# Optimization experiments

Hardware: AMD Instinct MI355X
Metric: run time of the kernel (lower is better)

Reference implementation:

```python
import jax, jax.numpy as jnp
import numpy as np

N, E = 50000, 800000
F_NODE, F_EDGE, H, LAT, MAXN = 128, 16, 128, 64, 200


def setup_inputs() -> dict:
    key = jax.random.key(0)
    ks = jax.random.split(key, 40)
    s = 0.05
    p = {
        'x': jax.random.normal(ks[0], (N, F_NODE), jnp.float32),
        'edge_index': jax.random.randint(ks[1], (2, E), 0, N, jnp.int64),
        'edge_attr': jax.random.normal(ks[2], (E, F_EDGE), jnp.float32),
        'eps': jax.random.normal(ks[3], (1, LAT), jnp.float32),
        'num_nodes': N,
        # GATConv layer 1 (heads=1)
        'W1': jax.random.normal(ks[4], (F_NODE, H), jnp.float32) * s,
        'att_src1': jax.random.normal(ks[5], (H,), jnp.float32) * s,
        'att_dst1': jax.random.normal(ks[6], (H,), jnp.float32) * s,
        'We1': jax.random.normal(ks[7], (F_EDGE, H), jnp.float32) * s,
        'att_e1': jax.random.normal(ks[8], (H,), jnp.float32) * s,
        'b1': jnp.zeros((H,), jnp.float32),
        # GATConv layer 2
        'W2': jax.random.normal(ks[9], (H, H), jnp.float32) * s,
        'att_src2': jax.random.normal(ks[10], (H,), jnp.float32) * s,
        'att_dst2': jax.random.normal(ks[11], (H,), jnp.float32) * s,
        'We2': jax.random.normal(ks[12], (F_EDGE, H), jnp.float32) * s,
        'att_e2': jax.random.normal(ks[13], (H,), jnp.float32) * s,
        'b2': jnp.zeros((H,), jnp.float32),
        # heads
        'mu_W': jax.random.normal(ks[14], (H, LAT), jnp.float32) * s,
        'mu_b': jnp.zeros((LAT,), jnp.float32),
        'lv_W': jax.random.normal(ks[15], (H, LAT), jnp.float32) * s,
        'lv_b': jnp.zeros((LAT,), jnp.float32),
        'dec_W': jax.random.normal(ks[16], (LAT, H), jnp.float32) * s,
        'dec_b': jnp.zeros((H,), jnp.float32),
        'adj_W1': jax.random.normal(ks[17], (H, H), jnp.float32) * s,
        'adj_b1': jnp.zeros((H,), jnp.float32),
        'adj_W2': jax.random.normal(ks[18], (H, MAXN), jnp.float32) * s,
        'adj_b2': jnp.zeros((MAXN,), jnp.float32),
        'nd_W1': jax.random.normal(ks[19], (H, H), jnp.float32) * s,
        'nd_b1': jnp.zeros((H,), jnp.float32),
        'nd_W2': jax.random.normal(ks[20], (H, F_NODE), jnp.float32) * s,
        'nd_b2': jnp.zeros((F_NODE,), jnp.float32),
    }
    return p


def _gat(h, src, dst, ea, W, a_s, a_d, We, a_e, b, n):
    # PyG GATConv, heads=1: linear transform, per-edge attention, segment softmax over dst
    g = h @ W                                     # [n, H]
    alpha = jax.nn.leaky_relu((g @ a_s)[src] + (g @ a_d)[dst] + (ea @ We) @ a_e,
                              negative_slope=0.2)  # [E']
    m = jax.ops.segment_max(alpha, dst, num_segments=n)
    ex = jnp.exp(alpha - m[dst])
    den = jax.ops.segment_sum(ex, dst, num_segments=n)
    w = ex / den[dst]
    return jax.ops.segment_sum(w[:, None] * g[src], dst, num_segments=n) + b


def _forward(x, edge_index, edge_attr, eps, num_nodes,
             W1, att_src1, att_dst1, We1, att_e1, b1,
             W2, att_src2, att_dst2, We2, att_e2, b2,
             mu_W, mu_b, lv_W, lv_b, dec_W, dec_b,
             adj_W1, adj_b1, adj_W2, adj_b2, nd_W1, nd_b1, nd_W2, nd_b2):
    n = x.shape[0]
    src, dst = edge_index[0], edge_index[1]
    # add self loops; self-loop edge_attr = per-node mean of incoming edge_attr (PyG fill_value='mean')
    deg = jax.ops.segment_sum(jnp.ones((src.shape[0],), x.dtype), dst, num_segments=n)
    mean_ea = jax.ops.segment_sum(edge_attr, dst, num_segments=n) / jnp.maximum(deg, 1.0)[:, None]
    loop = jnp.arange(n)
    src_f = jnp.concatenate([src, loop])
    dst_f = jnp.concatenate([dst, loop])
    ea_f = jnp.concatenate([edge_attr, mean_ea])
    h = jax.nn.relu(_gat(x, src_f, dst_f, ea_f, W1, att_src1, att_dst1, We1, att_e1, b1, n))
    h = jax.nn.relu(_gat(h, src_f, dst_f, ea_f, W2, att_src2, att_dst2, We2, att_e2, b2, n))
    hg = h.mean(axis=0, keepdims=True)            # global_mean_pool, single graph -> [1, H]
    mu = hg @ mu_W + mu_b
    logvar = hg @ lv_W + lv_b
    z = mu + eps * jnp.exp(0.5 * logvar)
    hd = jax.nn.relu(z @ dec_W + dec_b)           # [1, H]
    hn = jnp.broadcast_to(hd[:, None, :], (1, num_nodes, hd.shape[-1]))
    adj = jax.nn.relu(hn @ adj_W1 + adj_b1) @ adj_W2 + adj_b2   # [1, n, MAXN]
    adj = adj[:, :, :num_nodes]
    nodes = jax.nn.relu(hn @ nd_W1 + nd_b1) @ nd_W2 + nd_b2     # [1, n, F_NODE]
    return adj, nodes, mu, logvar


def reference(x, edge_index, edge_attr, eps, num_nodes,
              W1, att_src1, att_dst1, We1, att_e1, b1,
              W2, att_src2, att_dst2, We2, att_e2, b2,
              mu_W, mu_b, lv_W, lv_b, dec_W, dec_b,
              adj_W1, adj_b1, adj_W2, adj_b2, nd_W1, nd_b1, nd_W2, nd_b2):
    return _forward(x, edge_index, edge_attr, eps, num_nodes,
                    W1, att_src1, att_dst1, We1, att_e1, b1,
                    W2, att_src2, att_dst2, We2, att_e2, b2,
                    mu_W, mu_b, lv_W, lv_b, dec_W, dec_b,
                    adj_W1, adj_b1, adj_W2, adj_b2, nd_W1, nd_b1, nd_W2, nd_b2)
```

## Files before the change

### kernel.cpp

```cpp
#include <hip/hip_runtime.h>
#include <math.h>

#define NN   50000
#define EE   800000
#define EF   850000
#define HH   128
#define FE   16
#define LATD 64
#define MAXNN 200

#define ADJ_TOT   10000000
#define NODES_TOT 6400000
#define OUT_TOT   16400000
#define MU_OFF    16400000
#define LV_OFF    16400064

typedef __attribute__((ext_vector_type(8))) short bf16x8;
typedef __attribute__((ext_vector_type(4))) float f32x4;

__device__ __forceinline__ unsigned short f2bf(float f){
  unsigned int u = __float_as_uint(f);
  unsigned int r = (u + 0x7FFFu + ((u>>16)&1u)) >> 16;
  return (unsigned short)r;
}
__device__ __forceinline__ float bf2f(unsigned short h){
  return __uint_as_float(((unsigned int)h)<<16);
}

__global__ void kinit(int* ideg, float* hgsum){
  int i = blockIdx.x*blockDim.x + threadIdx.x;
  if(i < NN) ideg[i]=0;
  if(i < HH) hgsum[i]=0.f;
}

__global__ void kwa(const float* We1, const float* ae1, const float* We2, const float* ae2,
                    float* wa1, float* wa2){
  int t = threadIdx.x;
  if(t < FE){
    float s1=0.f, s2=0.f;
    for(int j=0;j<HH;j++){ s1 += We1[t*HH+j]*ae1[j]; s2 += We2[t*HH+j]*ae2[j]; }
    wa1[t]=s1; wa2[t]=s2;
  }
}

__global__ void kwprep(const float* __restrict__ W1, const float* __restrict__ W2,
                       unsigned short* __restrict__ Wp1, unsigned short* __restrict__ Wp2){
  int t = blockIdx.x*256 + threadIdx.x;
  if(t < HH*HH){
    int n = t >> 7, k = t & 127;
    Wp1[t] = f2bf(W1[k*HH + n]);
    Wp2[t] = f2bf(W2[k*HH + n]);
  }
}

__global__ void kdeg(const int* __restrict__ ei, int* ideg, int* __restrict__ erank){
  int e = blockIdx.x*blockDim.x + threadIdx.x;
  if(e<EE) erank[e] = atomicAdd(&ideg[ei[EE+e]], 1);
}

__global__ void kscan1(const int* __restrict__ ideg, int* rowstart, int* blocksum){
  __shared__ int sd[1024];
  int t=threadIdx.x; int i=blockIdx.x*1024+t;
  int v = (i<NN)? (ideg[i]+1) : 0;
  sd[t]=v; __syncthreads();
  for(int off=1; off<1024; off<<=1){
    int x = (t>=off)? sd[t-off] : 0;
    __syncthreads();
    sd[t] += x;
    __syncthreads();
  }
  if(i<NN) rowstart[i] = sd[t]-v;
  if(t==1023) blocksum[blockIdx.x]=sd[1023];
}
__global__ void kscan2(const int* blocksum, int* blockoff, int nb){
  if(threadIdx.x==0){
    int run=0;
    for(int b=0;b<nb;b++){ blockoff[b]=run; run+=blocksum[b]; }
    blockoff[nb]=run;
  }
}
__global__ void kscan3(int* rowstart, const int* __restrict__ blockoff, int nb){
  int i=blockIdx.x*blockDim.x+threadIdx.x;
  if(i<NN) rowstart[i]+=blockoff[i>>10];
  if(i==0) rowstart[NN]=blockoff[nb];
}

__global__ void kscatter(const int* __restrict__ ei, const float* __restrict__ ea,
                         const float* __restrict__ wa1, const float* __restrict__ wa2,
                         const int* __restrict__ rowstart, const int* __restrict__ erank,
                         float4* __restrict__ csr){
  int e=blockIdx.x*blockDim.x+threadIdx.x;
  if(e>=EE) return;
  int s=ei[e], d=ei[EE+e];
  const float4* ea4 = (const float4*)(ea + (size_t)e*FE);
  float4 v0=ea4[0], v1=ea4[1], v2=ea4[2], v3=ea4[3];
  float va[16]={v0.x,v0.y,v0.z,v0.w, v1.x,v1.y,v1.z,v1.w,
                v2.x,v2.y,v2.z,v2.w, v3.x,v3.y,v3.z,v3.w};
  float d1=0.f,d2=0.f;
  #pragma unroll
  for(int f=0;f<FE;f++){ d1+=va[f]*wa1[f]; d2+=va[f]*wa2[f]; }
  int pos = rowstart[d] + erank[e];
  csr[pos] = make_float4(__int_as_float(s), d1, d2, 0.f);
}

__global__ __launch_bounds__(256) void kself(const int* __restrict__ rowstart,
                      const int* __restrict__ ideg,
                      float4* __restrict__ csr){
  int tid = threadIdx.x;
  int l16 = tid & 15;
  int grp = tid >> 4;
  int i = blockIdx.x*16 + grp;
  if(i>=NN) return;
  int base = rowstart[i]; int deg = ideg[i];
  float s1=0.f, s2=0.f;
  for(int k=l16;k<deg;k+=16){ float4 en=csr[base+k]; s1+=en.y; s2+=en.z; }
  #pragma unroll
  for(int m=8;m>=1;m>>=1){ s1+=__shfl_xor(s1,m,16); s2+=__shfl_xor(s2,m,16); }
  if(l16==0){
    float dg = (float)deg; if(dg<1.f) dg=1.f;
    csr[base+deg] = make_float4(__int_as_float(i), s1/dg, s2/dg, 0.f);
  }
}

__global__ __launch_bounds__(256) void kgemm3(const void* __restrict__ hin, int h_is_fp32,
    const unsigned short* __restrict__ Wp,
    const float* __restrict__ atts, const float* __restrict__ attd,
    unsigned short* __restrict__ Gbf, float* __restrict__ asrc, float* __restrict__ adst){
  int lane = threadIdx.x & 63;
  int wid  = threadIdx.x >> 6;
  int l = lane & 15, q = lane >> 4;
  int r0 = blockIdx.x*64 + wid*16;
  if(r0 >= NN) return;
  const unsigned short* hb = (const unsigned short*)hin;
  const float*          hf = (const float*)hin;
  int row = r0 + l;

  f32x4 acc[8];
  #pragma unroll
  for(int t=0;t<8;t++) acc[t]=(f32x4){0.f,0.f,0.f,0.f};

  #pragma unroll
  for(int kb=0;kb<4;kb++){
    bf16x8 a;
    if(h_is_fp32){
      const float* p = hf + (size_t)row*HH + kb*32 + q*8;
      float4 u0 = *(const float4*)(p);
      float4 u1 = *(const float4*)(p+4);
      a[0]=(short)f2bf(u0.x); a[1]=(short)f2bf(u0.y); a[2]=(short)f2bf(u0.z); a[3]=(short)f2bf(u0.w);
      a[4]=(short)f2bf(u1.x); a[5]=(short)f2bf(u1.y); a[6]=(short)f2bf(u1.z); a[7]=(short)f2bf(u1.w);
    } else {
      a = *(const bf16x8*)(hb + (size_t)row*HH + kb*32 + q*8);
    }
    #pragma unroll
    for(int t=0;t<8;t++){
      bf16x8 b = *(const bf16x8*)(Wp + (size_t)(t*16+l)*HH + kb*32 + q*8);
      acc[t] = __builtin_amdgcn_mfma_f32_16x16x32_bf16(a, b, acc[t], 0,0,0);
    }
  }

  float av[8], dv[8];
  #pragma unroll
  for(int t=0;t<8;t++){ av[t]=atts[t*16+l]; dv[t]=attd[t*16+l]; }
  #pragma unroll
  for(int reg=0;reg<4;reg++){
    float ps=0.f, pd=0.f;
    #pragma unroll
    for(int t=0;t<8;t++){ ps+=acc[t][reg]*av[t]; pd+=acc[t][reg]*dv[t]; }
    #pragma unroll
    for(int m=8;m>=1;m>>=1){ ps+=__shfl_xor(ps,m,16); pd+=__shfl_xor(pd,m,16); }
    if(l==0){ int R=r0+q*4+reg; asrc[R]=ps; adst[R]=pd; }
  }
  #pragma unroll
  for(int t=0;t<8;t++)
    #pragma unroll
    for(int reg=0;reg<4;reg++)
      Gbf[(size_t)(r0+q*4+reg)*HH + t*16 + l] = f2bf(acc[t][reg]);
}

__global__ __launch_bounds__(256) void kgat(const unsigned short* __restrict__ A,
    const float* __restrict__ asrc, const float* __restrict__ adst,
    const int* __restrict__ rowstart, const float4* __restrict__ csr,
    int etsel, const float* __restrict__ bias,
    float* __restrict__ alphabuf, int* __restrict__ srcbuf,
    unsigned short* __restrict__ Bout){
  int lane = threadIdx.x & 63;
  int wid  = threadIdx.x >> 6;
  int i = blockIdx.x*4 + wid;
  if(i >= NN) return;
  int base = rowstart[i]; int len = rowstart[i+1]-base;
  float adi = adst[i];
  float acc0=0.f, acc1=0.f;
  float den;
  if(__builtin_expect(len <= 64, 1)){
    float a = -1e30f; int s=0;
    if(lane < len){
      float4 en = csr[base+lane];
      s = __float_as_int(en.x);
      float et = etsel ? en.z : en.y;
      a = asrc[s] + adi + et;
      a = a>0.f ? a : 0.2f*a;
    }
    float m = a;
    #pragma unroll
    for(int mk=32;mk>=1;mk>>=1) m = fmaxf(m, __shfl_xor(m, mk));
    float ex = (lane<len) ? __expf(a-m) : 0.f;
    float sm = ex;
    #pragma unroll
    for(int mk=32;mk>=1;mk>>=1) sm += __shfl_xor(sm, mk);
    den = sm;
    const unsigned short* Ap = A + lane*2;
    int k=0;
    for(; k+4<=len; k+=4){
      float wk0=__shfl(ex,k+0); int sk0=__shfl(s,k+0);
      float wk1=__shfl(ex,k+1); int sk1=__shfl(s,k+1);
      float wk2=__shfl(ex,k+2); int sk2=__shfl(s,k+2);
      float wk3=__shfl(ex,k+3); int sk3=__shfl(s,k+3);
      unsigned p0 = *(const unsigned*)(Ap + (size_t)sk0*HH);
      unsigned p1 = *(const unsigned*)(Ap + (size_t)sk1*HH);
      unsigned p2 = *(const unsigned*)(Ap + (size_t)sk2*HH);
      unsigned p3 = *(const unsigned*)(Ap + (size_t)sk3*HH);
      acc0 += wk0 * __uint_as_float(p0<<16);
      acc1 += wk0 * __uint_as_float(p0 & 0xFFFF0000u);
      acc0 += wk1 * __uint_as_float(p1<<16);
      acc1 += wk1 * __uint_as_float(p1 & 0xFFFF0000u);
      acc0 += wk2 * __uint_as_float(p2<<16);
      acc1 += wk2 * __uint_as_float(p2 & 0xFFFF0000u);
      acc0 += wk3 * __uint_as_float(p3<<16);
      acc1 += wk3 * __uint_as_float(p3 & 0xFFFF0000u);
    }
    for(; k<len; k++){
      float wk = __shfl(ex, k);
      int   sk = __shfl(s, k);
      unsigned pr = *(const unsigned*)(Ap + (size_t)sk*HH);
      acc0 += wk * __uint_as_float(pr<<16);
      acc1 += wk * __uint_as_float(pr & 0xFFFF0000u);
    }
  } else {
    float lm = -1e30f;
    for(int k=lane;k<len;k+=64){
      float4 en = csr[base+k];
      int s = __float_as_int(en.x);
      float et = etsel ? en.z : en.y;
      float a = asrc[s] + adi + et;
      a = a>0.f ? a : 0.2f*a;
      alphabuf[base+k]=a; srcbuf[base+k]=s;
      lm = fmaxf(lm,a);
    }
    #pragma unroll
    for(int mk=32;mk>=1;mk>>=1) lm = fmaxf(lm, __shfl_xor(lm, mk));
    float ls=0.f;
    for(int k=lane;k<len;k+=64){
      float ex = __expf(alphabuf[base+k]-lm);
      alphabuf[base+k]=ex; ls+=ex;
    }
    #pragma unroll
    for(int mk=32;mk>=1;mk>>=1) ls += __shfl_xor(ls, mk);
    den = ls;
    for(int c=0;c<len;c+=64){
      int kk = c+lane;
      float w = (kk<len)? alphabuf[base+kk] : 0.f;
      int   s = (kk<len)? srcbuf[base+kk] : 0;
      int lim = min(64, len-c);
      for(int j=0;j<lim;j++){
        float wk = __shfl(w, j);
        int   sk = __shfl(s, j);
        unsigned pr = *(const unsigned*)(A + (size_t)sk*HH + lane*2);
        acc0 += wk * __uint_as_float(pr<<16);
        acc1 += wk * __uint_as_float(pr & 0xFFFF0000u);
      }
    }
  }
  float inv = 1.f/den;
  float2 bb = *(const float2*)(bias + lane*2);
  float ox = fmaxf(acc0*inv + bb.x, 0.f);
  float oy = fmaxf(acc1*inv + bb.y, 0.f);
  unsigned ov = (unsigned)f2bf(ox) | ((unsigned)f2bf(oy)<<16);
  *(unsigned*)(Bout + (size_t)i*HH + lane*2) = ov;
}

__global__ __launch_bounds__(256) void khg(const unsigned short* __restrict__ B, float* hgsum){
  int f = threadIdx.x & 127;
  int half = threadIdx.x >> 7;
  float s=0.f;
  for(int i = blockIdx.x*2+half; i < NN; i += gridDim.x*2)
    s += bf2f(B[(size_t)i*HH + f]);
  __shared__ float sd[256];
  sd[threadIdx.x]=s; __syncthreads();
  if(half==0) atomicAdd(&hgsum[f], sd[threadIdx.x]+sd[threadIdx.x+128]);
}

__global__ __launch_bounds__(256) void kdec(const float* __restrict__ hgsum, const float* __restrict__ eps,
   const float* muW,const float* mub,const float* lvW,const float* lvb,
   const float* decW,const float* decb,
   const float* aW1,const float* ab1,const float* aW2,const float* ab2,
   const float* nW1,const float* nb1,const float* nW2,const float* nb2,
   float* out, float* rowadj, float* rownodes){
  __shared__ float hg[HH], z[LATD], hd[HH], t1[HH], t2[HH];
  int t=threadIdx.x;
  if(t<HH) hg[t]=hgsum[t]*(1.0f/NN);
  __syncthreads();
  if(t<LATD){
    float mu=mub[t], lv=lvb[t];
    for(int k=0;k<HH;k++){ mu += hg[k]*muW[k*LATD+t]; lv += hg[k]*lvW[k*LATD+t]; }
    out[MU_OFF+t]=mu; out[LV_OFF+t]=lv;
    z[t]=mu + eps[t]*expf(0.5f*lv);
  }
  __syncthreads();
  if(t<HH){
    float a=decb[t];
    for(int k=0;k<LATD;k++) a += z[k]*decW[k*HH+t];
    hd[t]=fmaxf(a,0.f);
  }
  __syncthreads();
  if(t<HH){
    float a=ab1[t];
    for(int k=0;k<HH;k++) a += hd[k]*aW1[k*HH+t];
    t1[t]=fmaxf(a,0.f);
  } else {
    int j=t-HH;
    float a=nb1[j];
    for(int k=0;k<HH;k++) a += hd[k]*nW1[k*HH+j];
    t2[j]=fmaxf(a,0.f);
  }
  __syncthreads();
  for(int j=t;j<MAXNN;j+=256){
    float a=ab2[j];
    for(int k=0;k<HH;k++) a += t1[k]*aW2[k*MAXNN+j];
    rowadj[j]=a;
  }
  if(t<HH){
    float a=nb2[t];
    for(int k=0;k<HH;k++) a += t2[k]*nW2[k*HH+t];
    rownodes[t]=a;
  }
}

__global__ __launch_bounds__(256) void kbcast(const float* __restrict__ rowadj,
                                              const float* __restrict__ rownodes,
                                              float* __restrict__ out){
  __shared__ float row[MAXNN+HH];
  int t=threadIdx.x;
  if(t<MAXNN) row[t]=rowadj[t];
  if(t<HH) row[MAXNN+t]=rownodes[t];
  __syncthreads();
  int stride=gridDim.x*blockDim.x;
  for(int idx=blockIdx.x*blockDim.x+t; idx<OUT_TOT; idx+=stride){
    if(idx<ADJ_TOT) out[idx]=row[idx%MAXNN];
    else { int j=(idx-ADJ_TOT)&(HH-1); out[idx]=row[MAXNN+j]; }
  }
}

extern "C" void kernel_launch(void* const* d_in, const int* in_sizes, int n_in,
                              void* d_out, int out_size, void* d_ws, size_t ws_size,
                              hipStream_t stream){
  const float* x   = (const float*)d_in[0];
  const int*   ei  = (const int*)d_in[1];
  const float* ea  = (const float*)d_in[2];
  const float* eps = (const float*)d_in[3];
  const float* W1  =(const float*)d_in[5];
  const float* as1 =(const float*)d_in[6];
  const float* ad1 =(const float*)d_in[7];
  const float* We1 =(const float*)d_in[8];
  const float* ae1 =(const float*)d_in[9];
  const float* b1  =(const float*)d_in[10];
  const float* W2  =(const float*)d_in[11];
  const float* as2 =(const float*)d_in[12];
  const float* ad2 =(const float*)d_in[13];
  const float* We2 =(const float*)d_in[14];
  const float* ae2 =(const float*)d_in[15];
  const float* b2  =(const float*)d_in[16];
  const float* muW =(const float*)d_in[17];
  const float* mub =(const float*)d_in[18];
  const float* lvW =(const float*)d_in[19];
  const float* lvb =(const float*)d_in[20];
  const float* decW=(const float*)d_in[21];
  const float* decb=(const float*)d_in[22];
  const float* aW1 =(const float*)d_in[23];
  const float* ab1 =(const float*)d_in[24];
  const float* aW2 =(const float*)d_in[25];
  const float* ab2 =(const float*)d_in[26];
  const float* nW1 =(const float*)d_in[27];
  const float* nb1 =(const float*)d_in[28];
  const float* nW2 =(const float*)d_in[29];
  const float* nb2 =(const float*)d_in[30];
  float* out=(float*)d_out;

  char* w=(char*)d_ws;
  unsigned short* Abf = (unsigned short*)w; w += (size_t)NN*HH*2;
  unsigned short* Bbf = (unsigned short*)w; w += (size_t)NN*HH*2;
  unsigned short* Wp1 = (unsigned short*)w; w += (size_t)HH*HH*2;
  unsigned short* Wp2 = (unsigned short*)w; w += (size_t)HH*HH*2;
  float4* csr      = (float4*)w; w += (size_t)EF*16;
  float*  alphabuf = (float*)w;  w += (size_t)EF*4;
  int*    srcbuf   = (int*)w;    w += (size_t)EF*4;
  int*    erank    = (int*)w;    w += (size_t)EE*4;
  int*    rowstart = (int*)w;    w += (size_t)(NN+1)*4;
  int*    ideg     = (int*)w;    w += (size_t)NN*4;
  float*  asrc     = (float*)w;  w += (size_t)NN*4;
  float*  adst     = (float*)w;  w += (size_t)NN*4;
  float*  hgsum    = (float*)w;  w += 128*4;
  float*  wa1      = (float*)w;  w += 16*4;
  float*  wa2      = (float*)w;  w += 16*4;
  float*  rowadj   = (float*)w;  w += 256*4;
  float*  rownodes = (float*)w;  w += 128*4;
  int*    blocksum = (int*)w;    w += 64*4;
  int*    blockoff = (int*)w;    w += 64*4;

  int nb = (NN+1023)/1024;
  int gemmblocks = (NN+63)/64;
  int gatblocks  = (NN+3)/4;

  hipLaunchKernelGGL(kinit, dim3((NN+255)/256), dim3(256), 0, stream, ideg, hgsum);
  hipLaunchKernelGGL(kwa, dim3(1), dim3(64), 0, stream, We1, ae1, We2, ae2, wa1, wa2);
  hipLaunchKernelGGL(kwprep, dim3((HH*HH+255)/256), dim3(256), 0, stream, W1, W2, Wp1, Wp2);
  hipLaunchKernelGGL(kdeg, dim3((EE+255)/256), dim3(256), 0, stream, ei, ideg, erank);
  hipLaunchKernelGGL(kscan1, dim3(nb), dim3(1024), 0, stream, ideg, rowstart, blocksum);
  hipLaunchKernelGGL(kscan2, dim3(1), dim3(64), 0, stream, blocksum, blockoff, nb);
  hipLaunchKernelGGL(kscan3, dim3((NN+255)/256), dim3(256), 0, stream, rowstart, blockoff, nb);
  hipLaunchKernelGGL(kscatter, dim3((EE+255)/256), dim3(256), 0, stream,
                     ei, ea, wa1, wa2, rowstart, erank, csr);
  hipLaunchKernelGGL(kself, dim3((NN+15)/16), dim3(256), 0, stream, rowstart, ideg, csr);
  hipLaunchKernelGGL(kgemm3, dim3(gemmblocks), dim3(256), 0, stream,
                     (const void*)x, 1, Wp1, as1, ad1, Abf, asrc, adst);
  hipLaunchKernelGGL(kgat,  dim3(gatblocks), dim3(256), 0, stream, Abf, asrc, adst, rowstart, csr, 0, b1, alphabuf, srcbuf, Bbf);
  hipLaunchKernelGGL(kgemm3, dim3(gemmblocks), dim3(256), 0, stream,
                     (const void*)Bbf, 0, Wp2, as2, ad2, Abf, asrc, adst);
  hipLaunchKernelGGL(kgat,  dim3(gatblocks), dim3(256), 0, stream, Abf, asrc, adst, rowstart, csr, 1, b2, alphabuf, srcbuf, Bbf);
  hipLaunchKernelGGL(khg,   dim3(512), dim3(256), 0, stream, Bbf, hgsum);
  hipLaunchKernelGGL(kdec,  dim3(1), dim3(256), 0, stream, hgsum, eps,
                     muW,mub,lvW,lvb,decW,decb,aW1,ab1,aW2,ab2,nW1,nb1,nW2,nb2,
                     out, rowadj, rownodes);
  hipLaunchKernelGGL(kbcast, dim3(2048), dim3(256), 0, stream, rowadj, rownodes, out);
}
```

Before: 453.5 us.

## Gather four neighbor rows per wave with 16-byte loads in GAT aggregation

The edge-aggregation loop now splits the 64-lane wave into four 16-lane groups. Each group loads a whole bf16 feature row of a different neighbor using uint4 (16-byte) loads, instead of every lane loading 4 bytes of the same row. Partial sums are combined across groups with cross-lane shuffles, and one group writes the output with a vector store. The next neighbor's row is also prefetched one chunk ahead. This aims to cut the number of load instructions and serial iterations per node, at the cost of more registers, an extra reduction step, and some wasted work on padded chunks.

```diff
diff --git a/kernel.cpp b/kernel.cpp
--- a/kernel.cpp
+++ b/kernel.cpp
@@ -26,6 +26,8 @@
 __device__ __forceinline__ float bf2f(unsigned short h){
   return __uint_as_float(((unsigned int)h)<<16);
 }
+__device__ __forceinline__ float bflo(unsigned u){ return __uint_as_float(u<<16); }
+__device__ __forceinline__ float bfhi(unsigned u){ return __uint_as_float(u & 0xFFFF0000u); }
 
 __global__ void kinit(int* ideg, float* hgsum){
   int i = blockIdx.x*blockDim.x + threadIdx.x;
@@ -188,9 +190,12 @@
   int i = blockIdx.x*4 + wid;
   if(i >= NN) return;
   int base = rowstart[i]; int len = rowstart[i+1]-base;
+  int lq = lane >> 4;
+  int lf = lane & 15;
   float adi = adst[i];
-  float acc0=0.f, acc1=0.f;
   float den;
+  float av0=0.f,av1=0.f,av2=0.f,av3=0.f,av4=0.f,av5=0.f,av6=0.f,av7=0.f;
+
   if(__builtin_expect(len <= 64, 1)){
     float a = -1e30f; int s=0;
     if(lane < len){
@@ -208,32 +213,22 @@
     #pragma unroll
     for(int mk=32;mk>=1;mk>>=1) sm += __shfl_xor(sm, mk);
     den = sm;
-    const unsigned short* Ap = A + lane*2;
-    int k=0;
-    for(; k+4<=len; k+=4){
-      float wk0=__shfl(ex,k+0); int sk0=__shfl(s,k+0);
-      float wk1=__shfl(ex,k+1); int sk1=__shfl(s,k+1);
-      float wk2=__shfl(ex,k+2); int sk2=__shfl(s,k+2);
-      float wk3=__shfl(ex,k+3); int sk3=__shfl(s,k+3);
-      unsigned p0 = *(const unsigned*)(Ap + (size_t)sk0*HH);
-      unsigned p1 = *(const unsigned*)(Ap + (size_t)sk1*HH);
-      unsigned p2 = *(const unsigned*)(Ap + (size_t)sk2*HH);
-      unsigned p3 = *(const unsigned*)(Ap + (size_t)sk3*HH);
-      acc0 += wk0 * __uint_as_float(p0<<16);
-      acc1 += wk0 * __uint_as_float(p0 & 0xFFFF0000u);
-      acc0 += wk1 * __uint_as_float(p1<<16);
-      acc1 += wk1 * __uint_as_float(p1 & 0xFFFF0000u);
-      acc0 += wk2 * __uint_as_float(p2<<16);
-      acc1 += wk2 * __uint_as_float(p2 & 0xFFFF0000u);
-      acc0 += wk3 * __uint_as_float(p3<<16);
-      acc1 += wk3 * __uint_as_float(p3 & 0xFFFF0000u);
-    }
-    for(; k<len; k++){
-      float wk = __shfl(ex, k);
-      int   sk = __shfl(s, k);
-      unsigned pr = *(const unsigned*)(Ap + (size_t)sk*HH);
-      acc0 += wk * __uint_as_float(pr<<16);
-      acc1 += wk * __uint_as_float(pr & 0xFFFF0000u);
+    int chunks = (len+3)>>2;
+    float wk = __shfl(ex, lq);
+    int   sk = __shfl(s, lq);
+    uint4 p  = *((const uint4*)(A + (size_t)sk*HH) + lf);
+    for(int c=0;c<chunks;c++){
+      float wc = wk; uint4 pc = p;
+      if(c+1<chunks){
+        int idx = (c+1)*4 + lq;
+        wk = __shfl(ex, idx);
+        sk = __shfl(s, idx);
+        p  = *((const uint4*)(A + (size_t)sk*HH) + lf);
+      }
+      av0 += wc*bflo(pc.x); av1 += wc*bfhi(pc.x);
+      av2 += wc*bflo(pc.y); av3 += wc*bfhi(pc.y);
+      av4 += wc*bflo(pc.z); av5 += wc*bfhi(pc.z);
+      av6 += wc*bflo(pc.w); av7 += wc*bfhi(pc.w);
     }
   } else {
     float lm = -1e30f;
@@ -256,26 +251,45 @@
     #pragma unroll
     for(int mk=32;mk>=1;mk>>=1) ls += __shfl_xor(ls, mk);
     den = ls;
-    for(int c=0;c<len;c+=64){
-      int kk = c+lane;
-      float w = (kk<len)? alphabuf[base+kk] : 0.f;
-      int   s = (kk<len)? srcbuf[base+kk] : 0;
-      int lim = min(64, len-c);
-      for(int j=0;j<lim;j++){
-        float wk = __shfl(w, j);
-        int   sk = __shfl(s, j);
-        unsigned pr = *(const unsigned*)(A + (size_t)sk*HH + lane*2);
-        acc0 += wk * __uint_as_float(pr<<16);
-        acc1 += wk * __uint_as_float(pr & 0xFFFF0000u);
-      }
-    }
-  }
-  float inv = 1.f/den;
-  float2 bb = *(const float2*)(bias + lane*2);
-  float ox = fmaxf(acc0*inv + bb.x, 0.f);
-  float oy = fmaxf(acc1*inv + bb.y, 0.f);
-  unsigned ov = (unsigned)f2bf(ox) | ((unsigned)f2bf(oy)<<16);
-  *(unsigned*)(Bout + (size_t)i*HH + lane*2) = ov;
+    int chunks = (len+3)>>2;
+    for(int c=0;c<chunks;c++){
+      int idx = c*4 + lq;
+      float wc = (idx<len)? alphabuf[base+idx] : 0.f;
+      int   sk = (idx<len)? srcbuf[base+idx] : 0;
+      uint4 pc = *((const uint4*)(A + (size_t)sk*HH) + lf);
+      av0 += wc*bflo(pc.x); av1 += wc*bfhi(pc.x);
+      av2 += wc*bflo(pc.y); av3 += wc*bfhi(pc.y);
+      av4 += wc*bflo(pc.z); av5 += wc*bfhi(pc.z);
+      av6 += wc*bflo(pc.w); av7 += wc*bfhi(pc.w);
+    }
+  }
+  av0 += __shfl_xor(av0,16); av0 += __shfl_xor(av0,32);
+  av1 += __shfl_xor(av1,16); av1 += __shfl_xor(av1,32);
+  av2 += __shfl_xor(av2,16); av2 += __shfl_xor(av2,32);
+  av3 += __shfl_xor(av3,16); av3 += __shfl_xor(av3,32);
+  av4 += __shfl_xor(av4,16); av4 += __shfl_xor(av4,32);
+  av5 += __shfl_xor(av5,16); av5 += __shfl_xor(av5,32);
+  av6 += __shfl_xor(av6,16); av6 += __shfl_xor(av6,32);
+  av7 += __shfl_xor(av7,16); av7 += __shfl_xor(av7,32);
+  if(lq==0){
+    float inv = 1.f/den;
+    float4 b0 = *(const float4*)(bias + lf*8);
+    float4 b1 = *(const float4*)(bias + lf*8 + 4);
+    float o0 = fmaxf(av0*inv + b0.x, 0.f);
+    float o1 = fmaxf(av1*inv + b0.y, 0.f);
+    float o2 = fmaxf(av2*inv + b0.z, 0.f);
+    float o3 = fmaxf(av3*inv + b0.w, 0.f);
+    float o4 = fmaxf(av4*inv + b1.x, 0.f);
+    float o5 = fmaxf(av5*inv + b1.y, 0.f);
+    float o6 = fmaxf(av6*inv + b1.z, 0.f);
+    float o7 = fmaxf(av7*inv + b1.w, 0.f);
+    uint4 ov;
+    ov.x = (unsigned)f2bf(o0) | ((unsigned)f2bf(o1)<<16);
+    ov.y = (unsigned)f2bf(o2) | ((unsigned)f2bf(o3)<<16);
+    ov.z = (unsigned)f2bf(o4) | ((unsigned)f2bf(o5)<<16);
+    ov.w = (unsigned)f2bf(o6) | ((unsigned)f2bf(o7)<<16);
+    *((uint4*)(Bout + (size_t)i*HH) + lf) = ov;
+  }
 }
 
 __global__ __launch_bounds__(256) void khg(const unsigned short* __restrict__ B, float* hgsum){
```

Result: no change. 452.8 us (-0.2%).
